# Kernel optimization log

Measured on AMD Instinct MI355X. Metric: run time of the kernel, lower is better.

The kernel has to match this reference:

```python
import math
import jax, jax.numpy as jnp
import numpy as np

INIT_TEMPERATURE = 0.07
MAX_SCALE = 100.0
B, D = 16384, 256


def setup_inputs() -> dict:
    key = jax.random.key(0)
    k1, k2 = jax.random.split(key)
    z_schema = jax.random.normal(k1, (B, D), dtype=jnp.float32)
    z_seal = jax.random.normal(k2, (B, D), dtype=jnp.float32)
    logit_scale = jnp.asarray(math.log(1.0 / INIT_TEMPERATURE), dtype=jnp.float32)
    return {"z_schema": z_schema, "z_seal": z_seal, "logit_scale": logit_scale}


def reference(z_schema, z_seal, logit_scale):
    # scale = min(exp(logit_scale), max_scale)
    scale = jnp.minimum(jnp.exp(logit_scale), jnp.float32(MAX_SCALE))
    # logits[i, j] = <z_schema[i], z_seal[j]> * scale   (B, B)
    logits = jnp.einsum("id,jd->ij", z_schema, z_seal) * scale
    # cross-entropy with labels = arange(B): loss = mean(lse(row) - diag)
    diag = jnp.diagonal(logits)
    lse_rows = jax.nn.logsumexp(logits, axis=1)  # s2r direction
    lse_cols = jax.nn.logsumexp(logits, axis=0)  # r2s direction (logits.T rows)
    loss_s2r = jnp.mean(lse_rows - diag)
    loss_r2s = jnp.mean(lse_cols - diag)
    loss = (loss_s2r + loss_r2s) * 0.5
    return (loss, loss)
```

## Files before the change

kernel.cpp:

```cpp
#include <hip/hip_runtime.h>
#include <hip/hip_bf16.h>
#include <math.h>

#define B_N 16384
#define D_K 256
#define JS 8
#define JRANGE (B_N / JS)
#define TJ 32
#define NT (JRANGE / TJ)
#define TILE_BYTES (TJ * D_K * 2)

typedef __bf16 bf16x8 __attribute__((ext_vector_type(8)));
typedef float f32x16 __attribute__((ext_vector_type(16)));

__device__ __forceinline__ unsigned short f2bf(float x) {
  unsigned u = __float_as_uint(x);
  unsigned r = (u + 0x7fffu + ((u >> 16) & 1u)) >> 16;
  return (unsigned short)r;
}

__device__ __forceinline__ float fexp2(float x) {
#if __has_builtin(__builtin_amdgcn_exp2f)
  return __builtin_amdgcn_exp2f(x);
#else
  return exp2f(x);
#endif
}

__device__ __forceinline__ void load_lds16(const void* g, void* l) {
  __builtin_amdgcn_global_load_lds(
      (const __attribute__((address_space(1))) unsigned int*)g,
      (__attribute__((address_space(3))) unsigned int*)l, 16, 0, 0);
}

__global__ void convert_diag_kernel(const float* __restrict__ A, const float* __restrict__ Bm,
                                    const float* __restrict__ lsp,
                                    unsigned short* __restrict__ Abf,
                                    unsigned short* __restrict__ Bbf,
                                    float* __restrict__ diag) {
  const float c = fminf(expf(lsp[0]), 100.0f) * 1.4426950408889634f;
  const int tid = threadIdx.x;
  const int idx = (blockIdx.x * 256 + tid) * 4;
  float4 a = *(const float4*)(A + idx);
  float4 b = *(const float4*)(Bm + idx);
  ushort4 ua, ub;
  ua.x = f2bf(a.x); ua.y = f2bf(a.y); ua.z = f2bf(a.z); ua.w = f2bf(a.w);
  ub.x = f2bf(b.x * c); ub.y = f2bf(b.y * c); ub.z = f2bf(b.z * c); ub.w = f2bf(b.w * c);
  *(ushort4*)(Abf + idx) = ua;
  *(ushort4*)(Bbf + idx) = ub;
  float d = a.x * b.x + a.y * b.y + a.z * b.z + a.w * b.w;
#pragma unroll
  for (int off = 32; off; off >>= 1) d += __shfl_xor(d, off);
  if ((tid & 63) == 0) diag[blockIdx.x * 4 + (tid >> 6)] = d;
}

__device__ __forceinline__ void upd(float& m, float& s, const f32x16& a) {
  float x0 = fmaxf(fmaxf(a[0], a[1]), a[2]);
  float x1 = fmaxf(fmaxf(a[3], a[4]), a[5]);
  float x2 = fmaxf(fmaxf(a[6], a[7]), a[8]);
  float x3 = fmaxf(fmaxf(a[9], a[10]), a[11]);
  float x4 = fmaxf(fmaxf(a[12], a[13]), a[14]);
  float y0 = fmaxf(fmaxf(x0, x1), x2);
  float y1 = fmaxf(fmaxf(x3, x4), a[15]);
  float mn = fmaxf(m, fmaxf(y0, y1));
  s *= fexp2(m - mn);
  float p0 = fexp2(a[0] - mn), p1 = fexp2(a[1] - mn);
  float p2 = fexp2(a[2] - mn), p3 = fexp2(a[3] - mn);
  p0 += fexp2(a[4] - mn);  p1 += fexp2(a[5] - mn);
  p2 += fexp2(a[6] - mn);  p3 += fexp2(a[7] - mn);
  p0 += fexp2(a[8] - mn);  p1 += fexp2(a[9] - mn);
  p2 += fexp2(a[10] - mn); p3 += fexp2(a[11] - mn);
  p0 += fexp2(a[12] - mn); p1 += fexp2(a[13] - mn);
  p2 += fexp2(a[14] - mn); p3 += fexp2(a[15] - mn);
  s += (p0 + p1) + (p2 + p3);
  m = mn;
}

__global__ __launch_bounds__(256, 2) void lse_kernel(const unsigned short* __restrict__ Abf,
                                                     const unsigned short* __restrict__ Bbf,
                                                     float* __restrict__ pm,
                                                     float* __restrict__ ps) {
  __shared__ __align__(16) unsigned char lds[2][TILE_BYTES];
  const int bid = blockIdx.x;
  const int dir = bid >> 9;
  const int iblk = (bid >> 3) & 63;
  const int js = bid & 7;
  const unsigned short* X = dir ? Bbf : Abf;
  const unsigned short* Y = dir ? Abf : Bbf;
  const int i0 = iblk * 256;
  const int j0 = js * JRANGE;
  const int w = threadIdx.x >> 6;
  const int l = threadIdx.x & 63;
  const int lc = l & 31, lh = l >> 5;

  bf16x8 xf0[16], xf1[16];
  {
    const unsigned short* Xr0 = X + (size_t)(i0 + w * 64 + lc) * D_K + lh * 8;
#pragma unroll
    for (int kk = 0; kk < 16; ++kk) {
      xf0[kk] = *(const bf16x8*)(Xr0 + kk * 16);
      xf1[kk] = *(const bf16x8*)(Xr0 + 32 * D_K + kk * 16);
    }
  }

  float m0 = -INFINITY, s0 = 0.f, m1 = -INFINITY, s1 = 0.f;

  const unsigned short* srcs[4];
  unsigned dsts[4];
#pragma unroll
  for (int r = 0; r < 4; ++r) {
    const int row = w * 8 + 2 * r + lh;
    srcs[r] = Y + (size_t)(j0 + row) * D_K + ((lc ^ (row & 7)) << 3);
    dsts[r] = w * 4096 + r * 1024;
  }

#define STAGE(bufidx)                                  \
  {                                                    \
    _Pragma("unroll") for (int r = 0; r < 4; ++r) {    \
      load_lds16(srcs[r], &lds[bufidx][dsts[r]]);      \
      srcs[r] += TJ * D_K;                             \
    }                                                  \
  }

  const unsigned vb = (unsigned)lc * 512 + ((unsigned)(lh ^ (lc & 7)) << 4);

#define CONSUME(bufidx)                                                          \
  {                                                                             \
    f32x16 acc0 = {};                                                           \
    f32x16 acc1 = {};                                                           \
    const unsigned char* lb = &lds[bufidx][0];                                  \
    __builtin_amdgcn_s_setprio(1);                                              \
    _Pragma("unroll") for (int kk = 0; kk < 16; ++kk) {                         \
      bf16x8 y = *(const bf16x8*)(lb + (vb ^ (unsigned)(kk << 5)));             \
      acc0 = __builtin_amdgcn_mfma_f32_32x32x16_bf16(y, xf0[kk], acc0, 0, 0, 0);\
      acc1 = __builtin_amdgcn_mfma_f32_32x32x16_bf16(y, xf1[kk], acc1, 0, 0, 0);\
    }                                                                           \
    __builtin_amdgcn_s_setprio(0);                                              \
    upd(m0, s0, acc0);                                                          \
    upd(m1, s1, acc1);                                                          \
  }

  STAGE(0);
  for (int t = 0; t < NT; t += 2) {
    __syncthreads();
    if (t + 1 < NT) STAGE(1);
    CONSUME(0);
    __syncthreads();
    if (t + 2 < NT) STAGE(0);
    CONSUME(1);
  }
#undef STAGE
#undef CONSUME

  {
    float mo = __shfl_xor(m0, 32), so = __shfl_xor(s0, 32);
    float mn = fmaxf(m0, mo);
    s0 = s0 * fexp2(m0 - mn) + so * fexp2(mo - mn); m0 = mn;
    mo = __shfl_xor(m1, 32); so = __shfl_xor(s1, 32);
    mn = fmaxf(m1, mo);
    s1 = s1 * fexp2(m1 - mn) + so * fexp2(mo - mn); m1 = mn;
  }

  if (lh == 0) {
    const int base = js * (2 * B_N) + dir * B_N + i0 + w * 64 + lc;
    pm[base] = m0;      ps[base] = s0;
    pm[base + 32] = m1; ps[base + 32] = s1;
  }
}

__global__ void combine_kernel(const float* __restrict__ pm, const float* __restrict__ ps,
                               float* __restrict__ lse) {
  int id = blockIdx.x * 256 + threadIdx.x;
  float m = -INFINITY, s = 0.f;
#pragma unroll
  for (int p = 0; p < JS; ++p) {
    float mo = pm[p * (2 * B_N) + id], so = ps[p * (2 * B_N) + id];
    float mn = fmaxf(m, mo);
    s = s * fexp2(m - mn) + so * fexp2(mo - mn);
    m = mn;
  }
  lse[id] = 0.6931471805599453f * (m + log2f(s));
}

__global__ void final_kernel(const float* __restrict__ lse, const float* __restrict__ diag,
                             const float* __restrict__ lsp, float* __restrict__ out) {
  const float scale = fminf(expf(lsp[0]), 100.0f);
  float part = 0.f;
  for (int i = threadIdx.x; i < B_N; i += 1024)
    part += 0.5f * (lse[i] + lse[B_N + i]) - scale * diag[i];
  __shared__ float red[1024];
  red[threadIdx.x] = part;
  __syncthreads();
  for (int off = 512; off; off >>= 1) {
    if (threadIdx.x < off) red[threadIdx.x] += red[threadIdx.x + off];
    __syncthreads();
  }
  if (threadIdx.x == 0) {
    float loss = red[0] / (float)B_N;
    out[0] = loss;
    out[1] = loss;
  }
}

extern "C" void kernel_launch(void* const* d_in, const int* in_sizes, int n_in,
                              void* d_out, int out_size, void* d_ws, size_t ws_size,
                              hipStream_t stream) {
  const float* A  = (const float*)d_in[0];
  const float* Bm = (const float*)d_in[1];
  const float* ls = (const float*)d_in[2];
  float* out = (float*)d_out;

  char* ws = (char*)d_ws;
  unsigned short* Abf = (unsigned short*)ws;
  unsigned short* Bbf = Abf + (size_t)B_N * D_K;
  float* diagp = (float*)(ws + 2ull * B_N * D_K * 2);
  float* lsep  = diagp + B_N;
  float* pm    = lsep + 2 * B_N;
  float* ps    = pm + JS * 2 * B_N;

  convert_diag_kernel<<<4096, 256, 0, stream>>>(A, Bm, ls, Abf, Bbf, diagp);
  lse_kernel<<<1024, 256, 0, stream>>>(Abf, Bbf, pm, ps);
  combine_kernel<<<128, 256, 0, stream>>>(pm, ps, lsep);
  final_kernel<<<1, 1024, 0, stream>>>(lsep, diagp, ls, out);
}
```

Baseline: 314.2 us.

## Software-pipeline MFMA tiles with exp/LSE updates using double accumulators

Splits each tile's MFMA chain into two halves and interleaves the online logsumexp update of the previous tile's accumulators between them. Two pairs of accumulators ping-pong so that MFMA and exp/VALU work can overlap within a wave. The prologue and epilogue are restructured accordingly and the setprio calls are dropped. This adds 32 accumulator registers, which risks register pressure or spills under launch_bounds(256,2).

```diff
diff --git a/kernel.cpp b/kernel.cpp
--- a/kernel.cpp
+++ b/kernel.cpp
@@ -54,7 +54,7 @@
   if ((tid & 63) == 0) diag[blockIdx.x * 4 + (tid >> 6)] = d;
 }
 
-__device__ __forceinline__ void upd(float& m, float& s, const f32x16& a) {
+__device__ __forceinline__ void upd(float& m, float& s, f32x16& a) {
   float x0 = fmaxf(fmaxf(a[0], a[1]), a[2]);
   float x1 = fmaxf(fmaxf(a[3], a[4]), a[5]);
   float x2 = fmaxf(fmaxf(a[6], a[7]), a[8]);
@@ -74,6 +74,7 @@
   p2 += fexp2(a[14] - mn); p3 += fexp2(a[15] - mn);
   s += (p0 + p1) + (p2 + p3);
   m = mn;
+  a = (f32x16){};
 }
 
 __global__ __launch_bounds__(256, 2) void lse_kernel(const unsigned short* __restrict__ Abf,
@@ -104,6 +105,7 @@
   }
 
   float m0 = -INFINITY, s0 = 0.f, m1 = -INFINITY, s1 = 0.f;
+  f32x16 accA0 = {}, accA1 = {}, accB0 = {}, accB1 = {};
 
   const unsigned short* srcs[4];
   unsigned dsts[4];
@@ -124,33 +126,43 @@
 
   const unsigned vb = (unsigned)lc * 512 + ((unsigned)(lh ^ (lc & 7)) << 4);
 
-#define CONSUME(bufidx)                                                          \
-  {                                                                             \
-    f32x16 acc0 = {};                                                           \
-    f32x16 acc1 = {};                                                           \
-    const unsigned char* lb = &lds[bufidx][0];                                  \
-    __builtin_amdgcn_s_setprio(1);                                              \
-    _Pragma("unroll") for (int kk = 0; kk < 16; ++kk) {                         \
-      bf16x8 y = *(const bf16x8*)(lb + (vb ^ (unsigned)(kk << 5)));             \
-      acc0 = __builtin_amdgcn_mfma_f32_32x32x16_bf16(y, xf0[kk], acc0, 0, 0, 0);\
-      acc1 = __builtin_amdgcn_mfma_f32_32x32x16_bf16(y, xf1[kk], acc1, 0, 0, 0);\
-    }                                                                           \
-    __builtin_amdgcn_s_setprio(0);                                              \
-    upd(m0, s0, acc0);                                                          \
-    upd(m1, s1, acc1);                                                          \
-  }
+#define HALF(bufidx, c0, c1, kklo)                                              \
+  {                                                                            \
+    const unsigned char* lb = &lds[bufidx][0];                                 \
+    _Pragma("unroll") for (int kk = (kklo); kk < (kklo) + 8; ++kk) {           \
+      bf16x8 y = *(const bf16x8*)(lb + (vb ^ (unsigned)(kk << 5)));            \
+      c0 = __builtin_amdgcn_mfma_f32_32x32x16_bf16(y, xf0[kk], c0, 0, 0, 0);   \
+      c1 = __builtin_amdgcn_mfma_f32_32x32x16_bf16(y, xf1[kk], c1, 0, 0, 0);   \
+    }                                                                          \
+  }
+
+#define CPIPE(bufidx, c0, c1, p0, p1) \
+  HALF(bufidx, c0, c1, 0);            \
+  upd(m0, s0, p0);                    \
+  HALF(bufidx, c0, c1, 8);            \
+  upd(m1, s1, p1);
 
   STAGE(0);
-  for (int t = 0; t < NT; t += 2) {
+  __syncthreads();
+  STAGE(1);
+  HALF(0, accA0, accA1, 0);
+  HALF(0, accA0, accA1, 8);
+  __syncthreads();
+
+  for (int t = 1; t < NT - 1; t += 2) {
+    STAGE(0);
+    CPIPE(1, accB0, accB1, accA0, accA1);
     __syncthreads();
-    if (t + 1 < NT) STAGE(1);
-    CONSUME(0);
+    STAGE(1);
+    CPIPE(0, accA0, accA1, accB0, accB1);
     __syncthreads();
-    if (t + 2 < NT) STAGE(0);
-    CONSUME(1);
-  }
+  }
+  CPIPE(1, accB0, accB1, accA0, accA1);
+  upd(m0, s0, accB0);
+  upd(m1, s1, accB1);
 #undef STAGE
-#undef CONSUME
+#undef HALF
+#undef CPIPE
 
   {
     float mo = __shfl_xor(m0, 32), so = __shfl_xor(s0, 32);
```

Result: slower. 440.6 us (+40.2%).

## Double LDS tile rows per stage and fold final reduction into combine

Applied to the files above, without the earlier changes.

Raises the Y tile staged into LDS per barrier from 32 to 64 rows, so each half of the double buffer feeds two MFMA sub-tiles. This halves the number of __syncthreads and stage rounds. LDS addressing now uses precomputed swizzled base pointers plus constant offsets. The combine kernel now also subtracts the diagonal term, reduces within each block and atomically accumulates into a scalar, leaving a trivial single-thread final kernel. It adds a memset, and doubling LDS use to 64 KB per block may limit residency under the 2-blocks-per-CU launch bound.

```diff
diff --git a/kernel.cpp b/kernel.cpp
--- a/kernel.cpp
+++ b/kernel.cpp
@@ -6,7 +6,7 @@
 #define D_K 256
 #define JS 8
 #define JRANGE (B_N / JS)
-#define TJ 32
+#define TJ 64
 #define NT (JRANGE / TJ)
 #define TILE_BYTES (TJ * D_K * 2)
 
@@ -105,49 +105,57 @@
 
   float m0 = -INFINITY, s0 = 0.f, m1 = -INFINITY, s1 = 0.f;
 
-  const unsigned short* srcs[4];
-  unsigned dsts[4];
-#pragma unroll
-  for (int r = 0; r < 4; ++r) {
-    const int row = w * 8 + 2 * r + lh;
+  const unsigned short* srcs[8];
+#pragma unroll
+  for (int r = 0; r < 8; ++r) {
+    const int row = w * 16 + 2 * r + lh;
     srcs[r] = Y + (size_t)(j0 + row) * D_K + ((lc ^ (row & 7)) << 3);
-    dsts[r] = w * 4096 + r * 1024;
-  }
-
-#define STAGE(bufidx)                                  \
-  {                                                    \
-    _Pragma("unroll") for (int r = 0; r < 4; ++r) {    \
-      load_lds16(srcs[r], &lds[bufidx][dsts[r]]);      \
-      srcs[r] += TJ * D_K;                             \
-    }                                                  \
+  }
+
+#define STAGE(bufidx)                                           \
+  {                                                             \
+    _Pragma("unroll") for (int r = 0; r < 8; ++r) {             \
+      load_lds16(srcs[r], &lds[bufidx][w * 8192 + r * 1024]);   \
+      srcs[r] += TJ * D_K;                                      \
+    }                                                           \
   }
 
   const unsigned vb = (unsigned)lc * 512 + ((unsigned)(lh ^ (lc & 7)) << 4);
-
-#define CONSUME(bufidx)                                                          \
-  {                                                                             \
-    f32x16 acc0 = {};                                                           \
-    f32x16 acc1 = {};                                                           \
-    const unsigned char* lb = &lds[bufidx][0];                                  \
-    __builtin_amdgcn_s_setprio(1);                                              \
-    _Pragma("unroll") for (int kk = 0; kk < 16; ++kk) {                         \
-      bf16x8 y = *(const bf16x8*)(lb + (vb ^ (unsigned)(kk << 5)));             \
+  const unsigned char* lb = &lds[0][0];
+  const unsigned char* bq0 = lb + (vb ^ 0u);
+  const unsigned char* bq1 = lb + (vb ^ 32u);
+  const unsigned char* bq2 = lb + (vb ^ 64u);
+  const unsigned char* bq3 = lb + (vb ^ 96u);
+
+#define CONSUME(bufidx, jh)                                                     \
+  {                                                                            \
+    f32x16 acc0 = {};                                                          \
+    f32x16 acc1 = {};                                                          \
+    __builtin_amdgcn_s_setprio(1);                                             \
+    _Pragma("unroll") for (int kk = 0; kk < 16; ++kk) {                        \
+      const unsigned char* bp = ((kk & 3) == 0) ? bq0                          \
+                              : ((kk & 3) == 1) ? bq1                          \
+                              : ((kk & 3) == 2) ? bq2 : bq3;                   \
+      bf16x8 y = *(const bf16x8*)(bp + (kk >> 2) * 128 + (jh)*16384 +          \
+                                  (bufidx)*32768);                             \
       acc0 = __builtin_amdgcn_mfma_f32_32x32x16_bf16(y, xf0[kk], acc0, 0, 0, 0);\
       acc1 = __builtin_amdgcn_mfma_f32_32x32x16_bf16(y, xf1[kk], acc1, 0, 0, 0);\
-    }                                                                           \
-    __builtin_amdgcn_s_setprio(0);                                              \
-    upd(m0, s0, acc0);                                                          \
-    upd(m1, s1, acc1);                                                          \
+    }                                                                          \
+    __builtin_amdgcn_s_setprio(0);                                             \
+    upd(m0, s0, acc0);                                                         \
+    upd(m1, s1, acc1);                                                         \
   }
 
   STAGE(0);
   for (int t = 0; t < NT; t += 2) {
     __syncthreads();
     if (t + 1 < NT) STAGE(1);
-    CONSUME(0);
+    CONSUME(0, 0);
+    CONSUME(0, 1);
     __syncthreads();
     if (t + 2 < NT) STAGE(0);
-    CONSUME(1);
+    CONSUME(1, 0);
+    CONSUME(1, 1);
   }
 #undef STAGE
 #undef CONSUME
@@ -169,8 +177,9 @@
 }
 
 __global__ void combine_kernel(const float* __restrict__ pm, const float* __restrict__ ps,
-                               float* __restrict__ lse) {
-  int id = blockIdx.x * 256 + threadIdx.x;
+                               const float* __restrict__ diag, const float* __restrict__ lsp,
+                               float* __restrict__ acc) {
+  const int id = blockIdx.x * 256 + threadIdx.x;
   float m = -INFINITY, s = 0.f;
 #pragma unroll
   for (int p = 0; p < JS; ++p) {
@@ -179,27 +188,26 @@
     s = s * fexp2(m - mn) + so * fexp2(mo - mn);
     m = mn;
   }
-  lse[id] = 0.6931471805599453f * (m + log2f(s));
-}
-
-__global__ void final_kernel(const float* __restrict__ lse, const float* __restrict__ diag,
-                             const float* __restrict__ lsp, float* __restrict__ out) {
-  const float scale = fminf(expf(lsp[0]), 100.0f);
-  float part = 0.f;
-  for (int i = threadIdx.x; i < B_N; i += 1024)
-    part += 0.5f * (lse[i] + lse[B_N + i]) - scale * diag[i];
-  __shared__ float red[1024];
-  red[threadIdx.x] = part;
+  float v = 0.5f * 0.6931471805599453f * (m + log2f(s));
+  if (id < B_N) {
+    const float scale = fminf(expf(lsp[0]), 100.0f);
+    v -= scale * diag[id];
+  }
+  __shared__ float red[256];
+  red[threadIdx.x] = v;
   __syncthreads();
-  for (int off = 512; off; off >>= 1) {
+#pragma unroll
+  for (int off = 128; off; off >>= 1) {
     if (threadIdx.x < off) red[threadIdx.x] += red[threadIdx.x + off];
     __syncthreads();
   }
-  if (threadIdx.x == 0) {
-    float loss = red[0] / (float)B_N;
-    out[0] = loss;
-    out[1] = loss;
-  }
+  if (threadIdx.x == 0) atomicAdd(acc, red[0]);
+}
+
+__global__ void final_kernel(const float* __restrict__ acc, float* __restrict__ out) {
+  float loss = acc[0] / (float)B_N;
+  out[0] = loss;
+  out[1] = loss;
 }
 
 extern "C" void kernel_launch(void* const* d_in, const int* in_sizes, int n_in,
@@ -214,12 +222,13 @@
   unsigned short* Abf = (unsigned short*)ws;
   unsigned short* Bbf = Abf + (size_t)B_N * D_K;
   float* diagp = (float*)(ws + 2ull * B_N * D_K * 2);
-  float* lsep  = diagp + B_N;
-  float* pm    = lsep + 2 * B_N;
+  float* pm    = diagp + B_N;
   float* ps    = pm + JS * 2 * B_N;
-
+  float* accp  = ps + JS * 2 * B_N;
+
+  hipMemsetAsync(accp, 0, sizeof(float), stream);
   convert_diag_kernel<<<4096, 256, 0, stream>>>(A, Bm, ls, Abf, Bbf, diagp);
   lse_kernel<<<1024, 256, 0, stream>>>(Abf, Bbf, pm, ps);
-  combine_kernel<<<128, 256, 0, stream>>>(pm, ps, lsep);
-  final_kernel<<<1, 1024, 0, stream>>>(lsep, diagp, ls, out);
-}
+  combine_kernel<<<128, 256, 0, stream>>>(pm, ps, diagp, ls, accp);
+  final_kernel<<<1, 1, 0, stream>>>(accp, out);
+}
```

Result: no change. 320.0 us (+1.9%).
